# Performance work log

Hardware: AMD Instinct MI355X
Metric: run time of the kernel (lower is better)

## Reference

```python
import jax, jax.numpy as jnp
import numpy as np

N_NODES = 32768
N_EDGES = 262144
HEAD = 8
CHANNEL = 64
LAYER_NUM = 2
HC = HEAD * CHANNEL  # 512


def setup_inputs() -> dict:
    key = jax.random.key(0)
    ks = jax.random.split(key, 12)
    def lin(k, fan_in, fan_out):
        s = 1.0 / np.sqrt(fan_in)
        kw, kb = jax.random.split(k)
        W = jax.random.uniform(kw, (fan_in, fan_out), jnp.float32, -s, s)
        b = jax.random.uniform(kb, (fan_out,), jnp.float32, -s, s)
        return W, b
    Wn, bn = lin(ks[0], 118, HC)
    We, be = lin(ks[1], 22, HC)
    Wa, ba = lin(ks[2], 2 * HC, HC)
    attn_w = jax.random.normal(ks[3], (1, HEAD, CHANNEL), jnp.float32) * 0.1
    x = jax.random.normal(ks[4], (N_NODES, 118), jnp.float32)
    edge_feat = jax.random.normal(ks[5], (N_EDGES, 22), jnp.float32)
    src = jax.random.randint(ks[6], (N_EDGES,), 0, N_NODES)
    dst = jax.random.randint(ks[7], (N_EDGES,), 0, N_NODES)
    return {"x": x, "edge_feat": edge_feat, "src": src, "dst": dst,
            "Wn": Wn, "bn": bn, "We": We, "be": be, "Wa": Wa, "ba": ba,
            "attn_w": attn_w}


def reference(x, edge_feat, src, dst, Wn, bn, We, be, Wa, ba, attn_w):
    N = x.shape[0]
    H, C = attn_w.shape[1], attn_w.shape[2]
    h = x @ Wn + bn                      # [N, H*C]
    _eh = edge_feat @ We + be            # computed in original forward, never used
    for _ in range(LAYER_NUM):
        # gather src/dst node states onto edges and score them (GATv2 style)
        e = jnp.concatenate([h[src], h[dst]], axis=-1)            # [E, 2HC]
        e = jax.nn.leaky_relu(e @ Wa + ba, negative_slope=0.01)   # [E, HC]
        score = jnp.sum(e.reshape(-1, H, C) * attn_w, axis=-1)    # [E, H]
        # edge softmax normalized over incoming edges of each dst node
        m = jax.ops.segment_max(score, dst, num_segments=N)       # [N, H]
        ex = jnp.exp(score - m[dst])                              # [E, H]
        denom = jax.ops.segment_sum(ex, dst, num_segments=N)      # [N, H]
        alpha = ex / denom[dst]                                   # [E, H]
        # weighted message passing: u_mul_e then sum over dst
        msg = h[src].reshape(-1, H, C) * alpha[:, :, None]        # [E, H, C]
        h = jax.ops.segment_sum(msg, dst, num_segments=N).reshape(N, H * C)
    return h
```

## Files before the change

### kernel.cpp

```cpp
#include <hip/hip_runtime.h>
#include <hip/hip_bf16.h>
#include <stdint.h>

#define N_NODES 32768
#define N_EDGES 262144

typedef __attribute__((ext_vector_type(8))) short short8;
typedef __attribute__((ext_vector_type(4))) float f32x4;
typedef __attribute__((ext_vector_type(4))) uint u32x4;

typedef const __attribute__((address_space(1))) void* gvp;
typedef __attribute__((address_space(3))) void* lvp;

__device__ __forceinline__ float bf2f(ushort u) {
  return __uint_as_float(((uint)u) << 16);
}
__device__ __forceinline__ ushort f2bf(float f) {
  uint x = __float_as_uint(f);
  uint r = (x + 0x7fffu + ((x >> 16) & 1u)) >> 16;
  return (ushort)r;
}
__device__ __forceinline__ float loadf(const void* p, size_t i, int isbf) {
  return isbf ? bf2f(((const ushort*)p)[i]) : ((const float*)p)[i];
}

__global__ void detect_dtype(const uint* __restrict__ xw, int* __restrict__ flag) {
  __shared__ int cnt;
  if (threadIdx.x == 0) cnt = 0;
  __syncthreads();
  int good = 0;
  for (int i = threadIdx.x; i < 1024; i += 256) {
    uint lo = xw[i] & 0xFFFFu;
    uint ef = (lo >> 7) & 0xFFu;
    if (lo == 0u || (ef >= 0x60u && ef <= 0x90u)) good++;
  }
  atomicAdd(&cnt, good);
  __syncthreads();
  if (threadIdx.x == 0) *flag = (cnt >= 614) ? 1 : 0;
}

__global__ void prep_all(const void* __restrict__ Wa, const void* __restrict__ Wn,
                         const void* __restrict__ ba, const void* __restrict__ bn,
                         const void* __restrict__ aw, const void* __restrict__ x,
                         const int* __restrict__ flag, const int* __restrict__ dst,
                         ushort* __restrict__ W2T, ushort* __restrict__ WnpT,
                         ushort* __restrict__ Wn_pad, float* __restrict__ bias2,
                         float* __restrict__ bnf, float* __restrict__ wf,
                         float* __restrict__ zbias, ushort* __restrict__ xp,
                         int* __restrict__ cnt) {
  const int b = blockIdx.x;
  if (b >= 2564 + 16384) {
    int e = (b - 2564 - 16384) * 256 + threadIdx.x;
    atomicAdd(&cnt[dst[e]], 1);
    return;
  }
  const int fl = *flag;
  if (b < 2048) {
    int t = b * 256 + threadIdx.x;
    int n = t >> 9, k = t & 511;
    size_t idx = (n < 512) ? ((size_t)k * 512 + n) : ((size_t)(512 + k) * 512 + (n - 512));
    W2T[t] = f2bf(loadf(Wa, idx, fl));
  } else if (b < 2304) {
    int t = (b - 2048) * 256 + threadIdx.x;
    int n = t >> 7, k = t & 127;
    WnpT[t] = (k < 118) ? f2bf(loadf(Wn, (size_t)k * 512 + n, fl)) : (ushort)0;
  } else if (b < 2560) {
    int t = (b - 2304) * 256 + threadIdx.x;
    int n = t >> 9, j = t & 511;
    Wn_pad[t] = (n < 118) ? f2bf(loadf(Wn, (size_t)n * 512 + j, fl)) : (ushort)0;
  } else if (b < 2564) {
    int t = (b - 2560) * 256 + threadIdx.x;
    if (t < 1024) bias2[t] = (t < 512) ? loadf(ba, t, fl) : 0.f;
    if (t < 512) { bnf[t] = loadf(bn, t, fl); wf[t] = loadf(aw, t, fl); }
    if (t < 128) zbias[t] = 0.f;
  } else {
    int t = (b - 2564) * 256 + threadIdx.x;
    int i = t >> 7, k = t & 127;
    xp[t] = (k < 118) ? f2bf(loadf(x, (size_t)i * 118 + k, fl)) : (ushort)0;
  }
}

__global__ __launch_bounds__(256)
void build_bc(const ushort* __restrict__ W2T, const float* __restrict__ bnf,
              const float* __restrict__ bias2, float* __restrict__ bc) {
  const int wave = threadIdx.x >> 6, lane = threadIdx.x & 63;
  const int j = blockIdx.x * 4 + wave;
  const uint4 v = *(const uint4*)(W2T + (size_t)j * 512 + lane * 8);
  const float4 b0 = *(const float4*)(bnf + lane * 8);
  const float4 b1 = *(const float4*)(bnf + lane * 8 + 4);
  const uint w[4] = {v.x, v.y, v.z, v.w};
  const float bb[8] = {b0.x, b0.y, b0.z, b0.w, b1.x, b1.y, b1.z, b1.w};
  float s = 0.f;
#pragma unroll
  for (int i = 0; i < 4; ++i) {
    s += __uint_as_float(w[i] << 16) * bb[2 * i];
    s += __uint_as_float(w[i] & 0xffff0000u) * bb[2 * i + 1];
  }
  s += __shfl_xor(s, 1);  s += __shfl_xor(s, 2);  s += __shfl_xor(s, 4);
  s += __shfl_xor(s, 8);  s += __shfl_xor(s, 16); s += __shfl_xor(s, 32);
  if (lane == 0) bc[j] = s + bias2[j];
}

__global__ __launch_bounds__(1024)
void csr_scan(const int* __restrict__ cnt, int* __restrict__ rowptr,
              int* __restrict__ cursor) {
  __shared__ int part[1024];
  const int t = threadIdx.x;
  const int base = t * 32;
  int loc[32];
  int s = 0;
#pragma unroll
  for (int i = 0; i < 32; ++i) { loc[i] = s; s += cnt[base + i]; }
  part[t] = s;
  __syncthreads();
  for (int off = 1; off < 1024; off <<= 1) {
    int v = (t >= off) ? part[t - off] : 0;
    __syncthreads();
    part[t] += v;
    __syncthreads();
  }
  int pre = (t == 0) ? 0 : part[t - 1];
#pragma unroll
  for (int i = 0; i < 32; ++i) {
    int v = pre + loc[i];
    rowptr[base + i] = v;
    cursor[base + i] = v;
  }
  if (t == 1023) rowptr[N_NODES] = part[1023];
}

__global__ void csr_fill(const int* __restrict__ dst, const int* __restrict__ src,
                         int* __restrict__ cursor, int* __restrict__ esrc) {
  int e = blockIdx.x * blockDim.x + threadIdx.x;
  int p = atomicAdd(&cursor[dst[e]], 1);
  esrc[p] = src[e];
}

__global__ __launch_bounds__(256)
void gemm_bf16(const ushort* __restrict__ A, const ushort* __restrict__ BT,
               const float* __restrict__ bias, ushort* __restrict__ C,
               int M, int N, int K) {
  __shared__ __align__(16) ushort As[128 * 32];
  __shared__ __align__(16) ushort Bs[128 * 32];
  const int tid = threadIdx.x, wave = tid >> 6, lane = tid & 63;
  const int bm = blockIdx.y * 128, bn = blockIdx.x * 128;
  const int wm = (wave >> 1) * 64, wn = (wave & 1) * 64;
  const int fcol = lane & 15, quad = lane >> 4;

  const f32x4 zero = {0.f, 0.f, 0.f, 0.f};
  f32x4 acc[4][4];
#pragma unroll
  for (int i = 0; i < 4; ++i)
#pragma unroll
    for (int j = 0; j < 4; ++j) acc[i][j] = zero;

  for (int k0 = 0; k0 < K; k0 += 32) {
#pragma unroll
    for (int r = 0; r < 2; ++r) {
      int o = r * 4096 + wave * 1024 + lane * 16;
      int row = o >> 6;
      int ke = (o & 63) >> 1;
      const ushort* gA = A + (size_t)(bm + row) * K + k0 + ke;
      const ushort* gB = BT + (size_t)(bn + row) * K + k0 + ke;
      ushort* lA = As + ((r * 4096 + wave * 1024) >> 1);
      ushort* lB = Bs + ((r * 4096 + wave * 1024) >> 1);
      __builtin_amdgcn_global_load_lds((gvp)(const void*)gA, (lvp)(void*)lA, 16, 0, 0);
      __builtin_amdgcn_global_load_lds((gvp)(const void*)gB, (lvp)(void*)lB, 16, 0, 0);
    }
    __syncthreads();
    short8 a[4], b[4];
#pragma unroll
    for (int i = 0; i < 4; ++i) {
      a[i] = *(const short8*)&As[(wm + i * 16 + fcol) * 32 + quad * 8];
      b[i] = *(const short8*)&Bs[(wn + i * 16 + fcol) * 32 + quad * 8];
    }
#pragma unroll
    for (int i = 0; i < 4; ++i)
#pragma unroll
      for (int j = 0; j < 4; ++j)
        acc[i][j] = __builtin_amdgcn_mfma_f32_16x16x32_bf16(a[i], b[j], acc[i][j], 0, 0, 0);
    __syncthreads();
  }

#pragma unroll
  for (int i = 0; i < 4; ++i) {
    int rowb = bm + wm + i * 16 + quad * 4;
#pragma unroll
    for (int j = 0; j < 4; ++j) {
      int col = bn + wn + j * 16 + fcol;
      float bb = bias[col];
#pragma unroll
      for (int r = 0; r < 4; ++r) {
        C[(size_t)(rowb + r) * N + col] = f2bf(acc[i][j][r] + bb);
      }
    }
  }
}

__global__ __launch_bounds__(256)
void node_fused_l1(const ushort* __restrict__ PQ1, const ushort* __restrict__ h0,
                   const int* __restrict__ esrc, const int* __restrict__ rowptr,
                   const float* __restrict__ wf, const float* __restrict__ bias2,
                   ushort* __restrict__ h1, ushort* __restrict__ PQ2) {
  const int wave = threadIdx.x >> 6, lane = threadIdx.x & 63;
  const int d = blockIdx.x * 4 + wave;
  const int beg = rowptr[d], end = rowptr[d + 1];
  const int c0 = lane * 8;

  const uint4 qv = *(const uint4*)(PQ1 + (size_t)d * 1024 + 512 + c0);
  const uint qw[4] = {qv.x, qv.y, qv.z, qv.w};
  float q[8], w[8];
#pragma unroll
  for (int i = 0; i < 4; ++i) {
    q[2 * i]     = __uint_as_float(qw[i] << 16);
    q[2 * i + 1] = __uint_as_float(qw[i] & 0xffff0000u);
  }
  const float4 w0 = *(const float4*)(wf + c0);
  const float4 w1 = *(const float4*)(wf + c0 + 4);
  w[0] = w0.x; w[1] = w0.y; w[2] = w0.z; w[3] = w0.w;
  w[4] = w1.x; w[5] = w1.y; w[6] = w1.z; w[7] = w1.w;

  float m = -3e38f, den = 0.f;
  float aP[8], aQ[8], aH[8];
#pragma unroll
  for (int i = 0; i < 8; ++i) { aP[i] = 0.f; aQ[i] = 0.f; aH[i] = 0.f; }

  if (beg < end) {
    int sj = esrc[beg];
    for (int j = beg; j < end; ++j) {
      const int s = sj;
      if (j + 1 < end) sj = esrc[j + 1];
      const uint4 pa = *(const uint4*)(PQ1 + (size_t)s * 1024 + c0);
      const uint4 pb = *(const uint4*)(PQ1 + (size_t)s * 1024 + 512 + c0);
      const uint4 hv = *(const uint4*)(h0 + (size_t)s * 512 + c0);
      const uint paw[4] = {pa.x, pa.y, pa.z, pa.w};
      const uint pbw[4] = {pb.x, pb.y, pb.z, pb.w};
      const uint hw[4]  = {hv.x, hv.y, hv.z, hv.w};
      float t = 0.f;
#pragma unroll
      for (int i = 0; i < 4; ++i) {
        float ea = __uint_as_float(paw[i] << 16) + q[2 * i];
        float eb = __uint_as_float(paw[i] & 0xffff0000u) + q[2 * i + 1];
        ea = (ea > 0.f) ? ea : 0.01f * ea;
        eb = (eb > 0.f) ? eb : 0.01f * eb;
        t += ea * w[2 * i] + eb * w[2 * i + 1];
      }
      t += __shfl_xor(t, 1);
      t += __shfl_xor(t, 2);
      t += __shfl_xor(t, 4);
      if (__any(t > m)) {
        const float mnew = fmaxf(m, t);
        const float corr = __expf(m - mnew);
        const float ex = __expf(t - mnew);
        den = den * corr + ex;
#pragma unroll
        for (int i = 0; i < 4; ++i) {
          aP[2 * i]     = aP[2 * i] * corr     + ex * __uint_as_float(paw[i] << 16);
          aP[2 * i + 1] = aP[2 * i + 1] * corr + ex * __uint_as_float(paw[i] & 0xffff0000u);
          aQ[2 * i]     = aQ[2 * i] * corr     + ex * __uint_as_float(pbw[i] << 16);
          aQ[2 * i + 1] = aQ[2 * i + 1] * corr + ex * __uint_as_float(pbw[i] & 0xffff0000u);
          aH[2 * i]     = aH[2 * i] * corr     + ex * __uint_as_float(hw[i] << 16);
          aH[2 * i + 1] = aH[2 * i + 1] * corr + ex * __uint_as_float(hw[i] & 0xffff0000u);
        }
        m = mnew;
      } else {
        const float ex = __expf(t - m);
        den += ex;
#pragma unroll
        for (int i = 0; i < 4; ++i) {
          aP[2 * i]     += ex * __uint_as_float(paw[i] << 16);
          aP[2 * i + 1] += ex * __uint_as_float(paw[i] & 0xffff0000u);
          aQ[2 * i]     += ex * __uint_as_float(pbw[i] << 16);
          aQ[2 * i + 1] += ex * __uint_as_float(pbw[i] & 0xffff0000u);
          aH[2 * i]     += ex * __uint_as_float(hw[i] << 16);
          aH[2 * i + 1] += ex * __uint_as_float(hw[i] & 0xffff0000u);
        }
      }
    }
  }

  const int deg = end - beg;
  const float inv = deg ? (1.f / den) : 0.f;
  const float4 bp0 = *(const float4*)(bias2 + c0);
  const float4 bp1 = *(const float4*)(bias2 + c0 + 4);
  const float bp[8] = {bp0.x, bp0.y, bp0.z, bp0.w, bp1.x, bp1.y, bp1.z, bp1.w};
  uint oP[4], oQ[4], oH[4];
#pragma unroll
  for (int i = 0; i < 4; ++i) {
    float p0 = deg ? aP[2 * i] * inv : bp[2 * i];
    float p1 = deg ? aP[2 * i + 1] * inv : bp[2 * i + 1];
    float q0 = deg ? aQ[2 * i] * inv : 0.f;
    float q1 = deg ? aQ[2 * i + 1] * inv : 0.f;
    float h0v = aH[2 * i] * inv, h1v = aH[2 * i + 1] * inv;
    oP[i] = (uint)f2bf(p0) | ((uint)f2bf(p1) << 16);
    oQ[i] = (uint)f2bf(q0) | ((uint)f2bf(q1) << 16);
    oH[i] = (uint)f2bf(h0v) | ((uint)f2bf(h1v) << 16);
  }
  u32x4 vP = {oP[0], oP[1], oP[2], oP[3]};
  u32x4 vQ = {oQ[0], oQ[1], oQ[2], oQ[3]};
  u32x4 vH = {oH[0], oH[1], oH[2], oH[3]};
  *(u32x4*)(PQ2 + (size_t)d * 1024 + c0) = vP;
  *(u32x4*)(PQ2 + (size_t)d * 1024 + 512 + c0) = vQ;
  *(u32x4*)(h1 + (size_t)d * 512 + c0) = vH;
}

__global__ __launch_bounds__(256)
void node_fused(const ushort* __restrict__ PQ, const ushort* __restrict__ hb_in,
                const int* __restrict__ esrc, const int* __restrict__ rowptr,
                const float* __restrict__ wf, const int* __restrict__ flag,
                ushort* __restrict__ hb_out, void* __restrict__ out, int write_out) {
  const int wave = threadIdx.x >> 6, lane = threadIdx.x & 63;
  const int d = blockIdx.x * 4 + wave;
  const int beg = rowptr[d], end = rowptr[d + 1];
  const int c0 = lane * 8;

  const uint4 qv = *(const uint4*)(PQ + (size_t)d * 1024 + 512 + c0);
  const uint qw[4] = {qv.x, qv.y, qv.z, qv.w};
  float q[8], w[8];
#pragma unroll
  for (int i = 0; i < 4; ++i) {
    q[2 * i]     = __uint_as_float(qw[i] << 16);
    q[2 * i + 1] = __uint_as_float(qw[i] & 0xffff0000u);
  }
  const float4 w0 = *(const float4*)(wf + c0);
  const float4 w1 = *(const float4*)(wf + c0 + 4);
  w[0] = w0.x; w[1] = w0.y; w[2] = w0.z; w[3] = w0.w;
  w[4] = w1.x; w[5] = w1.y; w[6] = w1.z; w[7] = w1.w;

  float m = -3e38f, den = 0.f;
  float acc[8] = {0.f, 0.f, 0.f, 0.f, 0.f, 0.f, 0.f, 0.f};

  if (beg < end) {
    int sj = esrc[beg];
    for (int j = beg; j < end; ++j) {
      const int s = sj;
      if (j + 1 < end) sj = esrc[j + 1];
      const uint4 pv = *(const uint4*)(PQ + (size_t)s * 1024 + c0);
      const uint4 hv = *(const uint4*)(hb_in + (size_t)s * 512 + c0);
      const uint pw[4] = {pv.x, pv.y, pv.z, pv.w};
      const uint hw[4] = {hv.x, hv.y, hv.z, hv.w};
      float t = 0.f;
#pragma unroll
      for (int i = 0; i < 4; ++i) {
        float ea = __uint_as_float(pw[i] << 16) + q[2 * i];
        float eb = __uint_as_float(pw[i] & 0xffff0000u) + q[2 * i + 1];
        ea = (ea > 0.f) ? ea : 0.01f * ea;
        eb = (eb > 0.f) ? eb : 0.01f * eb;
        t += ea * w[2 * i] + eb * w[2 * i + 1];
      }
      t += __shfl_xor(t, 1);
      t += __shfl_xor(t, 2);
      t += __shfl_xor(t, 4);
      if (__any(t > m)) {
        const float mnew = fmaxf(m, t);
        const float corr = __expf(m - mnew);
        const float ex = __expf(t - mnew);
        den = den * corr + ex;
#pragma unroll
        for (int i = 0; i < 4; ++i) {
          acc[2 * i]     = acc[2 * i] * corr     + ex * __uint_as_float(hw[i] << 16);
          acc[2 * i + 1] = acc[2 * i + 1] * corr + ex * __uint_as_float(hw[i] & 0xffff0000u);
        }
        m = mnew;
      } else {
        const float ex = __expf(t - m);
        den += ex;
#pragma unroll
        for (int i = 0; i < 4; ++i) {
          acc[2 * i]     += ex * __uint_as_float(hw[i] << 16);
          acc[2 * i + 1] += ex * __uint_as_float(hw[i] & 0xffff0000u);
        }
      }
    }
  }

  const float inv = (end > beg) ? (1.f / den) : 0.f;
  uint o[4];
#pragma unroll
  for (int i = 0; i < 4; ++i) {
    float v0 = acc[2 * i] * inv, v1 = acc[2 * i + 1] * inv;
    o[i] = (uint)f2bf(v0) | ((uint)f2bf(v1) << 16);
  }
  u32x4 ov = {o[0], o[1], o[2], o[3]};
  if (!write_out) {
    *(u32x4*)(hb_out + (size_t)d * 512 + c0) = ov;
  } else {
    if (*flag) {
      __builtin_nontemporal_store(ov, (u32x4*)((ushort*)out + (size_t)d * 512 + c0));
    } else {
      f32x4 f0 = {acc[0] * inv, acc[1] * inv, acc[2] * inv, acc[3] * inv};
      f32x4 f1 = {acc[4] * inv, acc[5] * inv, acc[6] * inv, acc[7] * inv};
      __builtin_nontemporal_store(f0, (f32x4*)((float*)out + (size_t)d * 512 + c0));
      __builtin_nontemporal_store(f1, (f32x4*)((float*)out + (size_t)d * 512 + c0 + 4));
    }
  }
}

extern "C" void kernel_launch(void* const* d_in, const int* in_sizes, int n_in,
                              void* d_out, int out_size, void* d_ws, size_t ws_size,
                              hipStream_t stream) {
  const void* x   = d_in[0];
  const int*  src = (const int*)d_in[2];
  const int*  dst = (const int*)d_in[3];
  const void* Wn  = d_in[4];
  const void* bn  = d_in[5];
  const void* Wa  = d_in[8];
  const void* ba  = d_in[9];
  const void* aw  = d_in[10];

  char* ws = (char*)d_ws;
  size_t off = 0;
  auto alloc = [&](size_t bytes) {
    char* p = ws + off;
    off = (off + bytes + 255) & ~(size_t)255;
    return p;
  };
  ushort* hbA    = (ushort*)alloc((size_t)N_NODES * 512 * 2);
  ushort* hbB    = (ushort*)alloc((size_t)N_NODES * 512 * 2);
  ushort* PQ     = (ushort*)alloc((size_t)N_NODES * 1024 * 2);
  int*    esrc   = (int*)   alloc((size_t)N_EDGES * 4);
  int*    rowptr = (int*)   alloc((size_t)(N_NODES + 1) * 4);
  int*    cnt    = (int*)   alloc((size_t)N_NODES * 4);
  int*    cursor = (int*)   alloc((size_t)N_NODES * 4);
  ushort* W2T    = (ushort*)alloc((size_t)1024 * 512 * 2);
  ushort* WcT    = (ushort*)alloc((size_t)1024 * 128 * 2);
  ushort* Wn_pad = (ushort*)alloc((size_t)128 * 512 * 2);
  float*  bias2  = (float*) alloc(1024 * 4);
  float*  bc     = (float*) alloc(1024 * 4);
  float*  zbias  = (float*) alloc(128 * 4);
  ushort* xp     = (ushort*)alloc((size_t)N_NODES * 128 * 2);
  ushort* WnpT   = (ushort*)alloc((size_t)512 * 128 * 2);
  float*  bnf    = (float*) alloc(512 * 4);
  float*  wf     = (float*) alloc(512 * 4);
  int*    flag   = (int*)   alloc(256);
  ushort* PQ2    = (ushort*)alloc((size_t)N_NODES * 1024 * 2);
  const bool fold = (off <= ws_size);

  detect_dtype<<<1, 256, 0, stream>>>((const uint*)x, flag);
  hipMemsetAsync(cnt, 0, (size_t)N_NODES * 4, stream);
  prep_all<<<2564 + 16384 + 1024, 256, 0, stream>>>(
      Wa, Wn, ba, bn, aw, x, flag, dst, W2T, WnpT, Wn_pad, bias2, bnf, wf, zbias,
      xp, cnt);
  build_bc<<<256, 256, 0, stream>>>(W2T, bnf, bias2, bc);
  {
    dim3 g(128 / 128, 1024 / 128);
    gemm_bf16<<<g, 256, 0, stream>>>(W2T, Wn_pad, zbias, WcT, 1024, 128, 512);
  }
  csr_scan<<<1, 1024, 0, stream>>>(cnt, rowptr, cursor);
  csr_fill<<<N_EDGES / 256, 256, 0, stream>>>(dst, src, cursor, esrc);

  {
    dim3 g(512 / 128, N_NODES / 128);
    gemm_bf16<<<g, 256, 0, stream>>>(xp, WnpT, bnf, hbA, N_NODES, 512, 128);
  }
  {
    dim3 g(1024 / 128, N_NODES / 128);
    gemm_bf16<<<g, 256, 0, stream>>>(xp, WcT, bc, PQ, N_NODES, 1024, 128);
  }

  if (fold) {
    node_fused_l1<<<N_NODES / 4, 256, 0, stream>>>(PQ, hbA, esrc, rowptr, wf,
                                                   bias2, hbB, PQ2);
    node_fused<<<N_NODES / 4, 256, 0, stream>>>(PQ2, hbB, esrc, rowptr, wf, flag,
                                                hbA, d_out, 1);
  } else {
    node_fused<<<N_NODES / 4, 256, 0, stream>>>(PQ, hbA, esrc, rowptr, wf, flag,
                                                hbB, d_out, 0);
    {
      dim3 g(1024 / 128, N_NODES / 128);
      gemm_bf16<<<g, 256, 0, stream>>>(hbB, W2T, bias2, PQ, N_NODES, 1024, 512);
    }
    node_fused<<<N_NODES / 4, 256, 0, stream>>>(PQ, hbB, esrc, rowptr, wf, flag,
                                                hbA, d_out, 1);
  }
}
```

Before: 434.8 us.

## Interleave h, P, Q per node into one row and merge node GEMMs

Packs the node state h and the projected P/Q halves into a single 1536-wide row per node. The two input GEMMs become one GEMM with a concatenated weight matrix and a combined bias. The gather kernels can then fetch all per-source data from one contiguous row, which improves locality and saves a launch. The unfolded fallback path is removed, so the code now assumes the workspace is large enough for both HP buffers.

```diff
diff --git a/kernel.cpp b/kernel.cpp
--- a/kernel.cpp
+++ b/kernel.cpp
@@ -11,6 +11,8 @@
 
 typedef const __attribute__((address_space(1))) void* gvp;
 typedef __attribute__((address_space(3))) void* lvp;
+
+#define LDH 1536
 
 __device__ __forceinline__ float bf2f(ushort u) {
   return __uint_as_float(((uint)u) << 16);
@@ -43,7 +45,7 @@
                          const void* __restrict__ ba, const void* __restrict__ bn,
                          const void* __restrict__ aw, const void* __restrict__ x,
                          const int* __restrict__ flag, const int* __restrict__ dst,
-                         ushort* __restrict__ W2T, ushort* __restrict__ WnpT,
+                         ushort* __restrict__ W2T, ushort* __restrict__ BTc,
                          ushort* __restrict__ Wn_pad, float* __restrict__ bias2,
                          float* __restrict__ bnf, float* __restrict__ wf,
                          float* __restrict__ zbias, ushort* __restrict__ xp,
@@ -63,7 +65,7 @@
   } else if (b < 2304) {
     int t = (b - 2048) * 256 + threadIdx.x;
     int n = t >> 7, k = t & 127;
-    WnpT[t] = (k < 118) ? f2bf(loadf(Wn, (size_t)k * 512 + n, fl)) : (ushort)0;
+    BTc[t] = (k < 118) ? f2bf(loadf(Wn, (size_t)k * 512 + n, fl)) : (ushort)0;
   } else if (b < 2560) {
     int t = (b - 2304) * 256 + threadIdx.x;
     int n = t >> 9, j = t & 511;
@@ -82,7 +84,9 @@
 
 __global__ __launch_bounds__(256)
 void build_bc(const ushort* __restrict__ W2T, const float* __restrict__ bnf,
-              const float* __restrict__ bias2, float* __restrict__ bc) {
+              const float* __restrict__ bias2, float* __restrict__ bcomb) {
+  const int tid = blockIdx.x * 256 + threadIdx.x;
+  if (tid < 512) bcomb[tid] = bnf[tid];
   const int wave = threadIdx.x >> 6, lane = threadIdx.x & 63;
   const int j = blockIdx.x * 4 + wave;
   const uint4 v = *(const uint4*)(W2T + (size_t)j * 512 + lane * 8);
@@ -98,7 +102,7 @@
   }
   s += __shfl_xor(s, 1);  s += __shfl_xor(s, 2);  s += __shfl_xor(s, 4);
   s += __shfl_xor(s, 8);  s += __shfl_xor(s, 16); s += __shfl_xor(s, 32);
-  if (lane == 0) bc[j] = s + bias2[j];
+  if (lane == 0) bcomb[512 + j] = s + bias2[j];
 }
 
 __global__ __launch_bounds__(1024)
@@ -139,7 +143,7 @@
 __global__ __launch_bounds__(256)
 void gemm_bf16(const ushort* __restrict__ A, const ushort* __restrict__ BT,
                const float* __restrict__ bias, ushort* __restrict__ C,
-               int M, int N, int K) {
+               int M, int N, int K, int lda, int ldc) {
   __shared__ __align__(16) ushort As[128 * 32];
   __shared__ __align__(16) ushort Bs[128 * 32];
   const int tid = threadIdx.x, wave = tid >> 6, lane = tid & 63;
@@ -160,7 +164,7 @@
       int o = r * 4096 + wave * 1024 + lane * 16;
       int row = o >> 6;
       int ke = (o & 63) >> 1;
-      const ushort* gA = A + (size_t)(bm + row) * K + k0 + ke;
+      const ushort* gA = A + (size_t)(bm + row) * lda + k0 + ke;
       const ushort* gB = BT + (size_t)(bn + row) * K + k0 + ke;
       ushort* lA = As + ((r * 4096 + wave * 1024) >> 1);
       ushort* lB = Bs + ((r * 4096 + wave * 1024) >> 1);
@@ -191,23 +195,22 @@
       float bb = bias[col];
 #pragma unroll
       for (int r = 0; r < 4; ++r) {
-        C[(size_t)(rowb + r) * N + col] = f2bf(acc[i][j][r] + bb);
+        C[(size_t)(rowb + r) * ldc + col] = f2bf(acc[i][j][r] + bb);
       }
     }
   }
 }
 
 __global__ __launch_bounds__(256)
-void node_fused_l1(const ushort* __restrict__ PQ1, const ushort* __restrict__ h0,
-                   const int* __restrict__ esrc, const int* __restrict__ rowptr,
-                   const float* __restrict__ wf, const float* __restrict__ bias2,
-                   ushort* __restrict__ h1, ushort* __restrict__ PQ2) {
+void node_fused_l1(const ushort* __restrict__ HP, const int* __restrict__ esrc,
+                   const int* __restrict__ rowptr, const float* __restrict__ wf,
+                   const float* __restrict__ bias2, ushort* __restrict__ HP2) {
   const int wave = threadIdx.x >> 6, lane = threadIdx.x & 63;
   const int d = blockIdx.x * 4 + wave;
   const int beg = rowptr[d], end = rowptr[d + 1];
   const int c0 = lane * 8;
 
-  const uint4 qv = *(const uint4*)(PQ1 + (size_t)d * 1024 + 512 + c0);
+  const uint4 qv = *(const uint4*)(HP + (size_t)d * LDH + 1024 + c0);
   const uint qw[4] = {qv.x, qv.y, qv.z, qv.w};
   float q[8], w[8];
 #pragma unroll
@@ -230,9 +233,10 @@
     for (int j = beg; j < end; ++j) {
       const int s = sj;
       if (j + 1 < end) sj = esrc[j + 1];
-      const uint4 pa = *(const uint4*)(PQ1 + (size_t)s * 1024 + c0);
-      const uint4 pb = *(const uint4*)(PQ1 + (size_t)s * 1024 + 512 + c0);
-      const uint4 hv = *(const uint4*)(h0 + (size_t)s * 512 + c0);
+      const ushort* row = HP + (size_t)s * LDH;
+      const uint4 hv = *(const uint4*)(row + c0);
+      const uint4 pa = *(const uint4*)(row + 512 + c0);
+      const uint4 pb = *(const uint4*)(row + 1024 + c0);
       const uint paw[4] = {pa.x, pa.y, pa.z, pa.w};
       const uint pbw[4] = {pb.x, pb.y, pb.z, pb.w};
       const uint hw[4]  = {hv.x, hv.y, hv.z, hv.w};
@@ -299,22 +303,22 @@
   u32x4 vP = {oP[0], oP[1], oP[2], oP[3]};
   u32x4 vQ = {oQ[0], oQ[1], oQ[2], oQ[3]};
   u32x4 vH = {oH[0], oH[1], oH[2], oH[3]};
-  *(u32x4*)(PQ2 + (size_t)d * 1024 + c0) = vP;
-  *(u32x4*)(PQ2 + (size_t)d * 1024 + 512 + c0) = vQ;
-  *(u32x4*)(h1 + (size_t)d * 512 + c0) = vH;
+  ushort* orow = HP2 + (size_t)d * LDH;
+  *(u32x4*)(orow + c0) = vH;
+  *(u32x4*)(orow + 512 + c0) = vP;
+  *(u32x4*)(orow + 1024 + c0) = vQ;
 }
 
 __global__ __launch_bounds__(256)
-void node_fused(const ushort* __restrict__ PQ, const ushort* __restrict__ hb_in,
-                const int* __restrict__ esrc, const int* __restrict__ rowptr,
-                const float* __restrict__ wf, const int* __restrict__ flag,
-                ushort* __restrict__ hb_out, void* __restrict__ out, int write_out) {
+void node_fused_l2(const ushort* __restrict__ HP2, const int* __restrict__ esrc,
+                   const int* __restrict__ rowptr, const float* __restrict__ wf,
+                   const int* __restrict__ flag, void* __restrict__ out) {
   const int wave = threadIdx.x >> 6, lane = threadIdx.x & 63;
   const int d = blockIdx.x * 4 + wave;
   const int beg = rowptr[d], end = rowptr[d + 1];
   const int c0 = lane * 8;
 
-  const uint4 qv = *(const uint4*)(PQ + (size_t)d * 1024 + 512 + c0);
+  const uint4 qv = *(const uint4*)(HP2 + (size_t)d * LDH + 1024 + c0);
   const uint qw[4] = {qv.x, qv.y, qv.z, qv.w};
   float q[8], w[8];
 #pragma unroll
@@ -335,8 +339,9 @@
     for (int j = beg; j < end; ++j) {
       const int s = sj;
       if (j + 1 < end) sj = esrc[j + 1];
-      const uint4 pv = *(const uint4*)(PQ + (size_t)s * 1024 + c0);
-      const uint4 hv = *(const uint4*)(hb_in + (size_t)s * 512 + c0);
+      const ushort* row = HP2 + (size_t)s * LDH;
+      const uint4 hv = *(const uint4*)(row + c0);
+      const uint4 pv = *(const uint4*)(row + 512 + c0);
       const uint pw[4] = {pv.x, pv.y, pv.z, pv.w};
       const uint hw[4] = {hv.x, hv.y, hv.z, hv.w};
       float t = 0.f;
@@ -375,24 +380,20 @@
   }
 
   const float inv = (end > beg) ? (1.f / den) : 0.f;
-  uint o[4];
-#pragma unroll
-  for (int i = 0; i < 4; ++i) {
-    float v0 = acc[2 * i] * inv, v1 = acc[2 * i + 1] * inv;
-    o[i] = (uint)f2bf(v0) | ((uint)f2bf(v1) << 16);
-  }
-  u32x4 ov = {o[0], o[1], o[2], o[3]};
-  if (!write_out) {
-    *(u32x4*)(hb_out + (size_t)d * 512 + c0) = ov;
+  if (*flag) {
+    uint o[4];
+#pragma unroll
+    for (int i = 0; i < 4; ++i) {
+      float v0 = acc[2 * i] * inv, v1 = acc[2 * i + 1] * inv;
+      o[i] = (uint)f2bf(v0) | ((uint)f2bf(v1) << 16);
+    }
+    u32x4 ov = {o[0], o[1], o[2], o[3]};
+    __builtin_nontemporal_store(ov, (u32x4*)((ushort*)out + (size_t)d * 512 + c0));
   } else {
-    if (*flag) {
-      __builtin_nontemporal_store(ov, (u32x4*)((ushort*)out + (size_t)d * 512 + c0));
-    } else {
-      f32x4 f0 = {acc[0] * inv, acc[1] * inv, acc[2] * inv, acc[3] * inv};
-      f32x4 f1 = {acc[4] * inv, acc[5] * inv, acc[6] * inv, acc[7] * inv};
-      __builtin_nontemporal_store(f0, (f32x4*)((float*)out + (size_t)d * 512 + c0));
-      __builtin_nontemporal_store(f1, (f32x4*)((float*)out + (size_t)d * 512 + c0 + 4));
-    }
+    f32x4 f0 = {acc[0] * inv, acc[1] * inv, acc[2] * inv, acc[3] * inv};
+    f32x4 f1 = {acc[4] * inv, acc[5] * inv, acc[6] * inv, acc[7] * inv};
+    __builtin_nontemporal_store(f0, (f32x4*)((float*)out + (size_t)d * 512 + c0));
+    __builtin_nontemporal_store(f1, (f32x4*)((float*)out + (size_t)d * 512 + c0 + 4));
   }
 }
 
@@ -415,62 +416,43 @@
     off = (off + bytes + 255) & ~(size_t)255;
     return p;
   };
-  ushort* hbA    = (ushort*)alloc((size_t)N_NODES * 512 * 2);
-  ushort* hbB    = (ushort*)alloc((size_t)N_NODES * 512 * 2);
-  ushort* PQ     = (ushort*)alloc((size_t)N_NODES * 1024 * 2);
+  ushort* HP     = (ushort*)alloc((size_t)N_NODES * LDH * 2);
+  ushort* HP2    = (ushort*)alloc((size_t)N_NODES * LDH * 2);
   int*    esrc   = (int*)   alloc((size_t)N_EDGES * 4);
   int*    rowptr = (int*)   alloc((size_t)(N_NODES + 1) * 4);
   int*    cnt    = (int*)   alloc((size_t)N_NODES * 4);
   int*    cursor = (int*)   alloc((size_t)N_NODES * 4);
   ushort* W2T    = (ushort*)alloc((size_t)1024 * 512 * 2);
-  ushort* WcT    = (ushort*)alloc((size_t)1024 * 128 * 2);
+  ushort* BTc    = (ushort*)alloc((size_t)1536 * 128 * 2);
   ushort* Wn_pad = (ushort*)alloc((size_t)128 * 512 * 2);
   float*  bias2  = (float*) alloc(1024 * 4);
-  float*  bc     = (float*) alloc(1024 * 4);
+  float*  bcomb  = (float*) alloc(1536 * 4);
   float*  zbias  = (float*) alloc(128 * 4);
   ushort* xp     = (ushort*)alloc((size_t)N_NODES * 128 * 2);
-  ushort* WnpT   = (ushort*)alloc((size_t)512 * 128 * 2);
   float*  bnf    = (float*) alloc(512 * 4);
   float*  wf     = (float*) alloc(512 * 4);
   int*    flag   = (int*)   alloc(256);
-  ushort* PQ2    = (ushort*)alloc((size_t)N_NODES * 1024 * 2);
-  const bool fold = (off <= ws_size);
 
   detect_dtype<<<1, 256, 0, stream>>>((const uint*)x, flag);
   hipMemsetAsync(cnt, 0, (size_t)N_NODES * 4, stream);
   prep_all<<<2564 + 16384 + 1024, 256, 0, stream>>>(
-      Wa, Wn, ba, bn, aw, x, flag, dst, W2T, WnpT, Wn_pad, bias2, bnf, wf, zbias,
+      Wa, Wn, ba, bn, aw, x, flag, dst, W2T, BTc, Wn_pad, bias2, bnf, wf, zbias,
       xp, cnt);
-  build_bc<<<256, 256, 0, stream>>>(W2T, bnf, bias2, bc);
+  build_bc<<<256, 256, 0, stream>>>(W2T, bnf, bias2, bcomb);
   {
     dim3 g(128 / 128, 1024 / 128);
-    gemm_bf16<<<g, 256, 0, stream>>>(W2T, Wn_pad, zbias, WcT, 1024, 128, 512);
+    gemm_bf16<<<g, 256, 0, stream>>>(W2T, Wn_pad, zbias, BTc + 512 * 128,
+                                     1024, 128, 512, 512, 128);
   }
   csr_scan<<<1, 1024, 0, stream>>>(cnt, rowptr, cursor);
   csr_fill<<<N_EDGES / 256, 256, 0, stream>>>(dst, src, cursor, esrc);
 
   {
-    dim3 g(512 / 128, N_NODES / 128);
-    gemm_bf16<<<g, 256, 0, stream>>>(xp, WnpT, bnf, hbA, N_NODES, 512, 128);
-  }
-  {
-    dim3 g(1024 / 128, N_NODES / 128);
-    gemm_bf16<<<g, 256, 0, stream>>>(xp, WcT, bc, PQ, N_NODES, 1024, 128);
-  }
-
-  if (fold) {
-    node_fused_l1<<<N_NODES / 4, 256, 0, stream>>>(PQ, hbA, esrc, rowptr, wf,
-                                                   bias2, hbB, PQ2);
-    node_fused<<<N_NODES / 4, 256, 0, stream>>>(PQ2, hbB, esrc, rowptr, wf, flag,
-                                                hbA, d_out, 1);
-  } else {
-    node_fused<<<N_NODES / 4, 256, 0, stream>>>(PQ, hbA, esrc, rowptr, wf, flag,
-                                                hbB, d_out, 0);
-    {
-      dim3 g(1024 / 128, N_NODES / 128);
-      gemm_bf16<<<g, 256, 0, stream>>>(hbB, W2T, bias2, PQ, N_NODES, 1024, 512);
-    }
-    node_fused<<<N_NODES / 4, 256, 0, stream>>>(PQ, hbB, esrc, rowptr, wf, flag,
-                                                hbA, d_out, 1);
-  }
-}
+    dim3 g(1536 / 128, N_NODES / 128);
+    gemm_bf16<<<g, 256, 0, stream>>>(xp, BTc, bcomb, HP,
+                                     N_NODES, 1536, 128, 128, LDH);
+  }
+
+  node_fused_l1<<<N_NODES / 4, 256, 0, stream>>>(HP, esrc, rowptr, wf, bias2, HP2);
+  node_fused_l2<<<N_NODES / 4, 256, 0, stream>>>(HP2, esrc, rowptr, wf, flag, d_out);
+}
```

Result: no change. 426.8 us (-1.8%).
